# Optimization experiments

Measured on AMD Instinct MI355X. Metric: run time of the kernel, lower is better.

The kernel has to match this reference:

```python
import jax, jax.numpy as jnp
import numpy as np

N = 100000      # nodes
E = 1600000     # edges
G = 8           # graphs in batch
H = 128         # hidden_dim
CNN = 768
MORPH = 6
NC = 5
EPS = 1e-5      # BatchNorm eps


def setup_inputs() -> dict:
    key = jax.random.key(0)
    ks = jax.random.split(key, 32)
    D = CNN + MORPH

    def w(k, shape, fan_in):
        # kaiming_normal_ (relu): std = sqrt(2/fan_in)
        return jax.random.normal(k, shape, jnp.float32) * np.sqrt(2.0 / fan_in)

    inp = {
        "cnn_features": jax.random.normal(ks[0], (N, CNN), jnp.float32),
        "morph_features": jax.random.normal(ks[1], (N, MORPH), jnp.float32),
        "cell_edge_index": jax.random.randint(ks[2], (2, E), 0, N, jnp.int32),
        "batch": jnp.sort(jax.random.randint(ks[3], (N,), 0, G, jnp.int32)),
        # GCN layers (weights stored [in, out])
        "gcn1_w": w(ks[4], (D, H), D), "gcn1_b": jnp.zeros((H,), jnp.float32),
        "gcn2_w": w(ks[5], (H, H), H), "gcn2_b": jnp.zeros((H,), jnp.float32),
        "gcn3_w": w(ks[6], (H, H), H), "gcn3_b": jnp.zeros((H,), jnp.float32),
        # BatchNorm affine params (eval mode, running_mean=0 running_var=1)
        "bn1_g": jnp.ones((H,), jnp.float32), "bn1_b": jnp.zeros((H,), jnp.float32),
        "bn2_g": jnp.ones((H,), jnp.float32), "bn2_b": jnp.zeros((H,), jnp.float32),
        "bn3_g": jnp.ones((H,), jnp.float32), "bn3_b": jnp.zeros((H,), jnp.float32),
        # attention gate: Linear(H,H) -> tanh -> Linear(H,1)
        "att_w1": w(ks[7], (H, H), H), "att_b1": jnp.zeros((H,), jnp.float32),
        "att_w2": w(ks[8], (H, 1), H), "att_b2": jnp.zeros((1,), jnp.float32),
        # classifier MLP
        "cls_w1": w(ks[9], (H, 2 * H), H), "cls_b1": jnp.zeros((2 * H,), jnp.float32),
        "cbn1_g": jnp.ones((2 * H,), jnp.float32), "cbn1_b": jnp.zeros((2 * H,), jnp.float32),
        "cls_w2": w(ks[10], (2 * H, H), 2 * H), "cls_b2": jnp.zeros((H,), jnp.float32),
        "cbn2_g": jnp.ones((H,), jnp.float32), "cbn2_b": jnp.zeros((H,), jnp.float32),
        "cls_w3": w(ks[11], (H, NC), H), "cls_b3": jnp.zeros((NC,), jnp.float32),
    }
    return inp


def _bn_eval(x, gamma, beta):
    # BatchNorm1d eval: running_mean=0, running_var=1
    return x * (gamma / np.sqrt(1.0 + EPS)) + beta


def _gcn(x, w, b, src, dst, dinv):
    h = x @ w                                   # [N, out]
    norm = dinv[src] * dinv[dst]                # [E]
    msg = h[src] * norm[:, None]                # [E, out]
    agg = jax.ops.segment_sum(msg, dst, num_segments=N)
    agg = agg + h * (dinv * dinv)[:, None]      # self-loop contribution
    return agg + b


def _forward(cnn_features, morph_features,
             gcn1_w, gcn1_b, gcn2_w, gcn2_b, gcn3_w, gcn3_b,
             bn1_g, bn1_b, bn2_g, bn2_b, bn3_g, bn3_b,
             att_w1, att_b1, att_w2, att_b2,
             cls_w1, cls_b1, cbn1_g, cbn1_b,
             cls_w2, cls_b2, cbn2_g, cbn2_b,
             cls_w3, cls_b3,
             cell_edge_index, batch):
    x = jnp.concatenate([cnn_features, morph_features], axis=1)  # [N, 774]
    src, dst = cell_edge_index[0], cell_edge_index[1]
    # symmetric GCN normalization with self-loops: deg = in-degree + 1
    deg = jax.ops.segment_sum(jnp.ones((E,), x.dtype), dst, num_segments=N) + 1.0
    dinv = jax.lax.rsqrt(deg)

    x1 = jax.nn.relu(_bn_eval(_gcn(x, gcn1_w, gcn1_b, src, dst, dinv), bn1_g, bn1_b))
    x2 = jax.nn.relu(_bn_eval(_gcn(x1, gcn2_w, gcn2_b, src, dst, dinv), bn2_g, bn2_b))
    x3 = jax.nn.relu(_bn_eval(_gcn(x2, gcn3_w, gcn3_b, src, dst, dinv), bn3_g, bn3_b))
    x_out = x1 + x2 + x3                                        # [N, H]

    # GlobalAttention pooling: segment softmax over per-graph nodes
    gate = jnp.tanh(x_out @ att_w1 + att_b1) @ att_w2 + att_b2  # [N, 1]
    gate = gate[:, 0]
    gmax = jax.ops.segment_max(gate, batch, num_segments=G)
    a = jnp.exp(gate - gmax[batch])
    denom = jax.ops.segment_sum(a, batch, num_segments=G)
    alpha = a / denom[batch]
    pooled = jax.ops.segment_sum(alpha[:, None] * x_out, batch, num_segments=G)  # [G, H]

    # classifier (dropout off, BN eval)
    h = jax.nn.relu(_bn_eval(pooled @ cls_w1 + cls_b1, cbn1_g, cbn1_b))
    h = jax.nn.relu(_bn_eval(h @ cls_w2 + cls_b2, cbn2_g, cbn2_b))
    return h @ cls_w3 + cls_b3                                  # [G, NC]


def reference(cnn_features, morph_features, cell_edge_index, batch,
              gcn1_w, gcn1_b, gcn2_w, gcn2_b, gcn3_w, gcn3_b,
              bn1_g, bn1_b, bn2_g, bn2_b, bn3_g, bn3_b,
              att_w1, att_b1, att_w2, att_b2,
              cls_w1, cls_b1, cbn1_g, cbn1_b,
              cls_w2, cls_b2, cbn2_g, cbn2_b,
              cls_w3, cls_b3):
    return _forward(cnn_features, morph_features,
                    gcn1_w, gcn1_b, gcn2_w, gcn2_b, gcn3_w, gcn3_b,
                    bn1_g, bn1_b, bn2_g, bn2_b, bn3_g, bn3_b,
                    att_w1, att_b1, att_w2, att_b2,
                    cls_w1, cls_b1, cbn1_g, cbn1_b,
                    cls_w2, cls_b2, cbn2_g, cbn2_b,
                    cls_w3, cls_b3,
                    cell_edge_index, batch)
```

## Files before the change

kernel.cpp:

```cpp
#include <hip/hip_runtime.h>
#include <hip/hip_bf16.h>

#define EPSV 1e-5f

typedef short short8v __attribute__((ext_vector_type(8)));
typedef float f32x4 __attribute__((ext_vector_type(4)));

__device__ __forceinline__ unsigned short f2bf(float f){
  unsigned u = __float_as_uint(f);
  unsigned r = u + 0x7fffu + ((u >> 16) & 1u);
  return (unsigned short)(r >> 16);
}
__device__ __forceinline__ unsigned pk2bf(float x, float y){
  return (unsigned)f2bf(x) | ((unsigned)f2bf(y) << 16);
}
__device__ __forceinline__ float bflo(unsigned u){ return __uint_as_float(u << 16); }
__device__ __forceinline__ float bfhi(unsigned u){ return __uint_as_float(u & 0xffff0000u); }

__device__ __forceinline__ unsigned enc_f(float f){
  unsigned u = __float_as_uint(f);
  return (u & 0x80000000u) ? ~u : (u | 0x80000000u);
}
__device__ __forceinline__ float dec_f(unsigned k){
  unsigned u = (k & 0x80000000u) ? (k & 0x7fffffffu) : ~k;
  return __uint_as_float(u);
}

__global__ void hist_kernel(const int* __restrict__ dst, int* __restrict__ deg, int E){
  int i = blockIdx.x*256 + threadIdx.x;
  if (i < E) atomicAdd(&deg[dst[i]], 1);
}

__global__ void scan_partial(const int* __restrict__ deg, int* __restrict__ bsums, int N){
  __shared__ int sd[256];
  int t = threadIdx.x;
  int base = blockIdx.x*1024 + t*4;
  int s = 0;
  if (base+0 < N) s += deg[base+0];
  if (base+1 < N) s += deg[base+1];
  if (base+2 < N) s += deg[base+2];
  if (base+3 < N) s += deg[base+3];
  sd[t]=s; __syncthreads();
  for (int off=128; off>0; off>>=1){
    if (t<off) sd[t]+=sd[t+off];
    __syncthreads();
  }
  if (t==0) bsums[blockIdx.x]=sd[0];
}

__global__ void scan_bsums(int* bsums, int* row_start, int B, int N, int E){
  if (threadIdx.x==0 && blockIdx.x==0){
    int run=0;
    for (int b=0;b<B;b++){ int v=bsums[b]; bsums[b]=run; run+=v; }
    row_start[N]=E;
  }
}

__global__ void scan_final(const int* __restrict__ deg, const int* __restrict__ bsums,
                           int* __restrict__ row_start, int* __restrict__ cursor, int N){
  __shared__ int sd[256];
  int t=threadIdx.x, b=blockIdx.x;
  int base=b*1024+t*4;
  int v0=0,v1=0,v2=0,v3=0;
  if (base+0<N) v0=deg[base+0];
  if (base+1<N) v1=deg[base+1];
  if (base+2<N) v2=deg[base+2];
  if (base+3<N) v3=deg[base+3];
  int s=v0+v1+v2+v3;
  sd[t]=s; __syncthreads();
  for (int off=1; off<256; off<<=1){
    int x = (t>=off)?sd[t-off]:0;
    __syncthreads();
    sd[t]+=x;
    __syncthreads();
  }
  int excl = sd[t]-s + bsums[b];
  int e0=excl, e1=excl+v0, e2=e1+v1, e3=e2+v2;
  if (base+0<N){ row_start[base+0]=e0; cursor[base+0]=e0; }
  if (base+1<N){ row_start[base+1]=e1; cursor[base+1]=e1; }
  if (base+2<N){ row_start[base+2]=e2; cursor[base+2]=e2; }
  if (base+3<N){ row_start[base+3]=e3; cursor[base+3]=e3; }
}

__global__ void dinv_kernel(const int* __restrict__ deg, float* __restrict__ dinv, int N){
  int i = blockIdx.x*256 + threadIdx.x;
  if (i < N) dinv[i] = rsqrtf((float)deg[i] + 1.0f);
}

__global__ void scatter_kernel(const int* __restrict__ src, const int* __restrict__ dst,
                               int* __restrict__ cursor, int* __restrict__ csr_src, int E){
  int i = blockIdx.x*256 + threadIdx.x;
  if (i < E){
    int d = dst[i];
    int pos = atomicAdd(&cursor[d], 1);
    csr_src[pos] = src[i];
  }
}

__global__ void wsplit_kernel(const float* __restrict__ W, unsigned short* __restrict__ WT,
                              int D, int Dpad){
  int k = blockIdx.x*256 + threadIdx.x;
  int c = blockIdx.y;
  if (k >= Dpad) return;
  float v = (k < D) ? W[(size_t)k*128 + c] : 0.f;
  WT[(size_t)c*Dpad + k] = f2bf(v);
}

__global__ __launch_bounds__(256, 4) void gemm_mfma_kernel(
    const float* __restrict__ xa, const float* __restrict__ xb,
    const unsigned short* __restrict__ WT,
    unsigned short* __restrict__ outb, int N, int Da, int Db, int Dpad)
{
  __shared__ unsigned short Abf[128*64];
  __shared__ unsigned short Bbf[128*64];

  const int tid  = threadIdx.x;
  const int lane = tid & 63;
  const int wave = tid >> 6;
  const int lr   = lane & 15;
  const int kg   = lane >> 4;
  const int rowBase = blockIdx.x * 128;
  const int D = Da + Db;

  f32x4 acc[2][8];
  #pragma unroll
  for (int s=0;s<2;s++)
    #pragma unroll
    for (int c=0;c<8;c++){ acc[s][c][0]=0.f; acc[s][c][1]=0.f; acc[s][c][2]=0.f; acc[s][c][3]=0.f; }

  const int arow = tid >> 1;
  const int akseg = (tid & 1) * 32;
  const int Rst = rowBase + arow;

  for (int kc = 0; kc < Dpad; kc += 64){
    __syncthreads();
    {
      const int gk0 = kc + akseg;
      const bool fastA = (Rst < N) && (gk0 + 32 <= Da);
      const int abase = arow*128 + akseg*2;
      const int aswz = (arow & 7) << 4;
      if (fastA){
        const float4* p4 = (const float4*)(xa + (size_t)Rst*Da + gk0);
        #pragma unroll
        for (int s=0;s<4;s++){
          float4 va = p4[2*s];
          float4 vb = p4[2*s+1];
          unsigned u[4];
          u[0] = pk2bf(va.x, va.y); u[1] = pk2bf(va.z, va.w);
          u[2] = pk2bf(vb.x, vb.y); u[3] = pk2bf(vb.z, vb.w);
          int off = (abase + s*16) ^ aswz;
          *(uint4*)((char*)Abf + off) = *(const uint4*)u;
        }
      } else {
        #pragma unroll
        for (int s=0;s<4;s++){
          unsigned u[4];
          #pragma unroll
          for (int q=0;q<4;q++){
            int gk = gk0 + s*8 + 2*q;
            float vx=0.f, vy=0.f;
            if (Rst < N){
              if (gk < Da) vx = xa[(size_t)Rst*Da + gk];
              else if (gk < D) vx = xb[(size_t)Rst*Db + (gk - Da)];
              if (gk+1 < Da) vy = xa[(size_t)Rst*Da + gk+1];
              else if (gk+1 < D) vy = xb[(size_t)Rst*Db + (gk+1 - Da)];
            }
            u[q] = pk2bf(vx, vy);
          }
          int off = (abase + s*16) ^ aswz;
          *(uint4*)((char*)Abf + off) = *(const uint4*)u;
        }
      }
    }
    {
      const unsigned short* ph = WT + (size_t)(tid>>1)*Dpad + kc + akseg;
      const int bbase = (tid>>1)*128 + akseg*2;
      const int bswz = ((tid>>1) & 7) << 4;
      #pragma unroll
      for (int s=0;s<4;s++){
        uint4 h = *(const uint4*)(ph + s*8);
        int off = (bbase + s*16) ^ bswz;
        *(uint4*)((char*)Bbf + off) = h;
      }
    }
    __syncthreads();
    #pragma unroll
    for (int ks=0; ks<2; ks++){
      const int kb = ks*64 + kg*16;
      const int r0 = wave*32 + lr;
      const int r1 = r0 + 16;
      const int offA0 = (r0*128 + kb) ^ ((r0&7)<<4);
      const int offA1 = (r1*128 + kb) ^ ((r1&7)<<4);
      short8v a0 = *(const short8v*)((const char*)Abf + offA0);
      short8v a1 = *(const short8v*)((const char*)Abf + offA1);
      #pragma unroll
      for (int ct=0; ct<8; ct++){
        const int c = ct*16 + lr;
        const int offB = (c*128 + kb) ^ ((c&7)<<4);
        short8v b = *(const short8v*)((const char*)Bbf + offB);
        acc[0][ct] = __builtin_amdgcn_mfma_f32_16x16x32_bf16(a0, b, acc[0][ct], 0,0,0);
        acc[1][ct] = __builtin_amdgcn_mfma_f32_16x16x32_bf16(a1, b, acc[1][ct], 0,0,0);
      }
    }
  }
  const int wrow = rowBase + wave*32;
  #pragma unroll
  for (int strip=0; strip<2; strip++){
    #pragma unroll
    for (int ct=0; ct<8; ct++){
      #pragma unroll
      for (int i=0;i<4;i++){
        int R = wrow + strip*16 + kg*4 + i;
        int C = ct*16 + lr;
        if (R < N) outb[(size_t)R*128 + C] = f2bf(acc[strip][ct][i]);
      }
    }
  }
}

#define ROWFMA(ACC, XV) \
  ACC.x = __builtin_fmaf((XV), w.x, ACC.x); \
  ACC.y = __builtin_fmaf((XV), w.y, ACC.y); \
  ACC.z = __builtin_fmaf((XV), w.z, ACC.z); \
  ACC.w = __builtin_fmaf((XV), w.w, ACC.w);

#define FMA_STEP(K) { \
  const float4 w   = *(const float4*)(Wl + (K)*128 + wb); \
  const float4 xlo = *(const float4*)(Xl + (K)*64 + r0); \
  const float4 xhi = *(const float4*)(Xl + (K)*64 + r0 + 4); \
  ROWFMA(acc0, xlo.x) ROWFMA(acc1, xlo.y) ROWFMA(acc2, xlo.z) ROWFMA(acc3, xlo.w) \
  ROWFMA(acc4, xhi.x) ROWFMA(acc5, xhi.y) ROWFMA(acc6, xhi.z) ROWFMA(acc7, xhi.w) }

#define GEMM_LOOP \
  const int tid  = threadIdx.x; \
  const int lane = tid & 63; \
  const int wave = tid >> 6; \
  const int half = lane >> 5; \
  const int ff   = lane & 31; \
  const int r0   = wave*16 + half*8; \
  const int wb   = ff << 2; \
  const int srow = tid >> 2; \
  const int skg  = (tid & 3) << 4; \
  const int R_s  = rowBase + srow; \
  float4 acc0={0,0,0,0},acc1={0,0,0,0},acc2={0,0,0,0},acc3={0,0,0,0}; \
  float4 acc4={0,0,0,0},acc5={0,0,0,0},acc6={0,0,0,0},acc7={0,0,0,0}; \
  for (int kc = 0; kc < D; kc += 64){ \
    const int L = (D - kc < 64) ? (D - kc) : 64; \
    __syncthreads(); \
    { \
      const int nf4 = (L*128) >> 2; \
      const float4* Wg = (const float4*)(W + (size_t)kc*128); \
      float4* Wl4 = (float4*)Wl; \
      for (int idx = tid; idx < nf4; idx += 256) Wl4[idx] = Wg[idx]; \
    } \
    if (L == 64 && kc + 64 <= Da){ \
      float4 v0={0,0,0,0},v1={0,0,0,0},v2={0,0,0,0},v3={0,0,0,0}; \
      if (R_s < N){ \
        const float4* xr = (const float4*)(xa + (size_t)R_s*Da + kc + skg); \
        v0 = xr[0]; v1 = xr[1]; v2 = xr[2]; v3 = xr[3]; \
      } \
      Xl[(skg+ 0)*64 + srow]=v0.x; Xl[(skg+ 1)*64 + srow]=v0.y; \
      Xl[(skg+ 2)*64 + srow]=v0.z; Xl[(skg+ 3)*64 + srow]=v0.w; \
      Xl[(skg+ 4)*64 + srow]=v1.x; Xl[(skg+ 5)*64 + srow]=v1.y; \
      Xl[(skg+ 6)*64 + srow]=v1.z; Xl[(skg+ 7)*64 + srow]=v1.w; \
      Xl[(skg+ 8)*64 + srow]=v2.x; Xl[(skg+ 9)*64 + srow]=v2.y; \
      Xl[(skg+10)*64 + srow]=v2.z; Xl[(skg+11)*64 + srow]=v2.w; \
      Xl[(skg+12)*64 + srow]=v3.x; Xl[(skg+13)*64 + srow]=v3.y; \
      Xl[(skg+14)*64 + srow]=v3.z; Xl[(skg+15)*64 + srow]=v3.w; \
    } else if (skg < L){ \
      const int lim = (L - skg < 16) ? (L - skg) : 16; \
      for (int i2=0;i2<lim;i2++){ \
        const int gk = kc + skg + i2; \
        float v = 0.f; \
        if (R_s < N) v = (gk < Da) ? xa[(size_t)R_s*Da + gk] \
                                   : xb[(size_t)R_s*Db + (gk - Da)]; \
        Xl[(skg+i2)*64 + srow] = v; \
      } \
    } \
    __syncthreads(); \
    if (L == 64){ \
      _Pragma("unroll 4") \
      for (int k=0;k<64;k++){ FMA_STEP(k) } \
    } else { \
      for (int k=0;k<L;k++){ FMA_STEP(k) } \
    } \
  }

__global__ __launch_bounds__(256) void att_kernel(
    const float* __restrict__ xa, const float* __restrict__ W,
    const float* __restrict__ b1, const float* __restrict__ w2,
    const float* __restrict__ b2, float* __restrict__ gate, int N)
{
  __shared__ float Wl[64*128];
  __shared__ float Xl[64*64];
  const int rowBase = blockIdx.x*64;
  const float* xb = xa;
  const int D = 128, Da = 128, Db = 0;
  GEMM_LOOP
  const int R0 = rowBase + r0;
  const float4 b1v = *(const float4*)(b1 + (ff<<2));
  const float4 w2v = *(const float4*)(w2 + (ff<<2));
  const float bias2 = b2[0];
#define ATT_ROW(ACC, RR) { \
    float p = tanhf(ACC.x + b1v.x)*w2v.x + tanhf(ACC.y + b1v.y)*w2v.y \
            + tanhf(ACC.z + b1v.z)*w2v.z + tanhf(ACC.w + b1v.w)*w2v.w; \
    p += __shfl_xor(p, 1);  p += __shfl_xor(p, 2); \
    p += __shfl_xor(p, 4);  p += __shfl_xor(p, 8); \
    p += __shfl_xor(p, 16); \
    if (ff == 0){ int R = R0 + (RR); if (R < N) gate[R] = p + bias2; } }
  ATT_ROW(acc0,0) ATT_ROW(acc1,1) ATT_ROW(acc2,2) ATT_ROW(acc3,3)
  ATT_ROW(acc4,4) ATT_ROW(acc5,5) ATT_ROW(acc6,6) ATT_ROW(acc7,7)
#undef ATT_ROW
}

__global__ __launch_bounds__(256) void gather_kernel(
    const unsigned short* __restrict__ hb, const float* __restrict__ dinv,
    const int* __restrict__ row_start, const int* __restrict__ csr_src,
    const float* __restrict__ bias, const float* __restrict__ bng, const float* __restrict__ bnb,
    const float* __restrict__ x1in, const float* __restrict__ x2in,
    float* __restrict__ out, int N, int mode)
{
  const int grp = (blockIdx.x * 256 + threadIdx.x) >> 4;
  const int sl  = threadIdx.x & 15;
  if (grp >= N) return;
  const int i = grp;
  const float di = dinv[i];

  float a[8];
  {
    uint4 u = *(const uint4*)(hb + (size_t)i*128 + sl*8);
    float w0 = di*di;
    a[0] = bflo(u.x)*w0; a[1] = bfhi(u.x)*w0;
    a[2] = bflo(u.y)*w0; a[3] = bfhi(u.y)*w0;
    a[4] = bflo(u.z)*w0; a[5] = bfhi(u.z)*w0;
    a[6] = bflo(u.w)*w0; a[7] = bfhi(u.w)*w0;
  }
  const int s0 = row_start[i], s1 = row_start[i+1];
  for (int base = s0; base < s1; base += 16){
    const int nloc = (s1 - base < 16) ? (s1 - base) : 16;
    int sv = 0; float nv = 0.f;
    if (sl < nloc){ sv = csr_src[base + sl]; nv = dinv[sv]*di; }
    for (int j=0;j<nloc;j++){
      int   sj = __shfl(sv, j, 16);
      float nj = __shfl(nv, j, 16);
      uint4 u = *(const uint4*)(hb + (size_t)sj*128 + sl*8);
      a[0] = __builtin_fmaf(bflo(u.x), nj, a[0]);
      a[1] = __builtin_fmaf(bfhi(u.x), nj, a[1]);
      a[2] = __builtin_fmaf(bflo(u.y), nj, a[2]);
      a[3] = __builtin_fmaf(bfhi(u.y), nj, a[3]);
      a[4] = __builtin_fmaf(bflo(u.z), nj, a[4]);
      a[5] = __builtin_fmaf(bfhi(u.z), nj, a[5]);
      a[6] = __builtin_fmaf(bflo(u.w), nj, a[6]);
      a[7] = __builtin_fmaf(bfhi(u.w), nj, a[7]);
    }
  }
  const int f0 = sl*8;
  const float bsc = rsqrtf(1.0f + EPSV);
  float4 bi0 = *(const float4*)(bias + f0);
  float4 bi1 = *(const float4*)(bias + f0 + 4);
  float4 g0 = *(const float4*)(bng + f0);
  float4 g1 = *(const float4*)(bng + f0 + 4);
  float4 be0 = *(const float4*)(bnb + f0);
  float4 be1 = *(const float4*)(bnb + f0 + 4);
  float v[8];
  v[0] = fmaxf(0.f, (a[0]+bi0.x)*(g0.x*bsc) + be0.x);
  v[1] = fmaxf(0.f, (a[1]+bi0.y)*(g0.y*bsc) + be0.y);
  v[2] = fmaxf(0.f, (a[2]+bi0.z)*(g0.z*bsc) + be0.z);
  v[3] = fmaxf(0.f, (a[3]+bi0.w)*(g0.w*bsc) + be0.w);
  v[4] = fmaxf(0.f, (a[4]+bi1.x)*(g1.x*bsc) + be1.x);
  v[5] = fmaxf(0.f, (a[5]+bi1.y)*(g1.y*bsc) + be1.y);
  v[6] = fmaxf(0.f, (a[6]+bi1.z)*(g1.z*bsc) + be1.z);
  v[7] = fmaxf(0.f, (a[7]+bi1.w)*(g1.w*bsc) + be1.w);
  if (mode == 2){
    float4 p0 = *(const float4*)(x1in + (size_t)i*128 + f0);
    float4 p1 = *(const float4*)(x1in + (size_t)i*128 + f0 + 4);
    float4 q0 = *(const float4*)(x2in + (size_t)i*128 + f0);
    float4 q1 = *(const float4*)(x2in + (size_t)i*128 + f0 + 4);
    v[0]+=p0.x+q0.x; v[1]+=p0.y+q0.y; v[2]+=p0.z+q0.z; v[3]+=p0.w+q0.w;
    v[4]+=p1.x+q1.x; v[5]+=p1.y+q1.y; v[6]+=p1.z+q1.z; v[7]+=p1.w+q1.w;
  }
  float4 o0; o0.x=v[0]; o0.y=v[1]; o0.z=v[2]; o0.w=v[3];
  float4 o1; o1.x=v[4]; o1.y=v[5]; o1.z=v[6]; o1.w=v[7];
  *(float4*)(out + (size_t)i*128 + f0)     = o0;
  *(float4*)(out + (size_t)i*128 + f0 + 4) = o1;
}

__global__ void segmax_kernel(const float* __restrict__ gate, const int* __restrict__ batch,
                              unsigned* __restrict__ mg, int N){
  __shared__ unsigned sm[8];
  int t = threadIdx.x;
  if (t < 8) sm[t] = 0u;
  __syncthreads();
  int i = blockIdx.x*256 + t;
  if (i < N) atomicMax(&sm[batch[i]], enc_f(gate[i]));
  __syncthreads();
  if (t < 8) atomicMax(&mg[t], sm[t]);
}

__global__ void expsum_kernel(const float* __restrict__ gate, const int* __restrict__ batch,
                              const unsigned* __restrict__ mg, float* __restrict__ aex,
                              float* __restrict__ denom, int N){
  __shared__ float sd[8];
  int t = threadIdx.x;
  if (t < 8) sd[t] = 0.f;
  __syncthreads();
  int i = blockIdx.x*256 + t;
  if (i < N){
    int g = batch[i];
    float m = dec_f(mg[g]);
    float av = expf(gate[i] - m);
    aex[i] = av;
    atomicAdd(&sd[g], av);
  }
  __syncthreads();
  if (t < 8) atomicAdd(&denom[t], sd[t]);
}

__global__ void pooled_kernel(const float* __restrict__ aex, const float* __restrict__ xo,
                              const int* __restrict__ batch, float* __restrict__ pooled, int N){
  int t = threadIdx.x;
  int hlf = t >> 7;
  int f = t & 127;
  int nb = gridDim.x;
  int per = (N + nb - 1)/nb;
  int start = blockIdx.x*per;
  int end = (N < start + per) ? N : (start + per);
  float acc = 0.f; int gcur = -1;
  for (int i = start + hlf; i < end; i += 2){
    int g = batch[i];
    if (g != gcur){
      if (gcur >= 0) atomicAdd(&pooled[gcur*128 + f], acc);
      acc = 0.f; gcur = g;
    }
    acc = __builtin_fmaf(aex[i], xo[(size_t)i*128 + f], acc);
  }
  if (gcur >= 0) atomicAdd(&pooled[gcur*128 + f], acc);
}

__global__ __launch_bounds__(256) void classifier_kernel(
    const float* __restrict__ pooled, const float* __restrict__ denom,
    const float* __restrict__ w1, const float* __restrict__ b1,
    const float* __restrict__ g1, const float* __restrict__ be1,
    const float* __restrict__ w2, const float* __restrict__ b2,
    const float* __restrict__ g2, const float* __restrict__ be2,
    const float* __restrict__ w3, const float* __restrict__ b3,
    float* __restrict__ outp)
{
  __shared__ float pl[8*128];
  __shared__ float h1[8*256];
  __shared__ float h2l[8*128];
  int t = threadIdx.x;
  for (int idx = t; idx < 1024; idx += 256){
    int g = idx >> 7;
    pl[idx] = pooled[idx] / denom[g];
  }
  __syncthreads();
  {
    float a0=0,a1=0,a2=0,a3=0,a4=0,a5=0,a6=0,a7=0;
    for (int k=0; k<128; k++){
      float w = w1[k*256 + t];
      a0 = __builtin_fmaf(pl[0*128+k], w, a0);
      a1 = __builtin_fmaf(pl[1*128+k], w, a1);
      a2 = __builtin_fmaf(pl[2*128+k], w, a2);
      a3 = __builtin_fmaf(pl[3*128+k], w, a3);
      a4 = __builtin_fmaf(pl[4*128+k], w, a4);
      a5 = __builtin_fmaf(pl[5*128+k], w, a5);
      a6 = __builtin_fmaf(pl[6*128+k], w, a6);
      a7 = __builtin_fmaf(pl[7*128+k], w, a7);
// ... 33 lines not shown
    h2l[5*128+t] = fmaxf(0.f, (a5+bb)*s + tb);
    h2l[6*128+t] = fmaxf(0.f, (a6+bb)*s + tb);
    h2l[7*128+t] = fmaxf(0.f, (a7+bb)*s + tb);
  }
  __syncthreads();
  if (t < 40){
    int g = t/5, c = t%5;
    float s = 0.f;
    for (int k=0; k<128; k++) s = __builtin_fmaf(h2l[g*128+k], w3[k*5+c], s);
    outp[t] = s + b3[c];
  }
}

extern "C" void kernel_launch(void* const* d_in, const int* in_sizes, int n_in,
                              void* d_out, int out_size, void* d_ws, size_t ws_size,
                              hipStream_t stream)
{
  const float* cnn   = (const float*)d_in[0];
  const float* morph = (const float*)d_in[1];
  const int*   eidx  = (const int*)d_in[2];
  const int*   batch = (const int*)d_in[3];
  const float* g1w = (const float*)d_in[4];
  const float* g1b = (const float*)d_in[5];
  const float* g2w = (const float*)d_in[6];
  const float* g2b = (const float*)d_in[7];
  const float* g3w = (const float*)d_in[8];
  const float* g3b = (const float*)d_in[9];
  const float* bn1g=(const float*)d_in[10], *bn1b=(const float*)d_in[11];
  const float* bn2g=(const float*)d_in[12], *bn2b=(const float*)d_in[13];
  const float* bn3g=(const float*)d_in[14], *bn3b=(const float*)d_in[15];
  const float* aw1=(const float*)d_in[16], *ab1=(const float*)d_in[17];
  const float* aw2=(const float*)d_in[18], *ab2=(const float*)d_in[19];
  const float* cw1=(const float*)d_in[20], *cb1=(const float*)d_in[21];
  const float* c1g=(const float*)d_in[22], *c1b=(const float*)d_in[23];
  const float* cw2=(const float*)d_in[24], *cb2=(const float*)d_in[25];
  const float* c2g=(const float*)d_in[26], *c2b=(const float*)d_in[27];
  const float* cw3=(const float*)d_in[28], *cb3=(const float*)d_in[29];

  const int N = in_sizes[3];
  const int E = in_sizes[2] / 2;
  const int CNNW = in_sizes[0] / N;
  const int MOR  = in_sizes[1] / N;
  const int D = CNNW + MOR;
  const int Dpad1 = ((D + 63)/64)*64;

  char* p = (char*)d_ws;
  auto alloc = [&](size_t bytes)->char* {
    char* r = p; p += (bytes + 255) & ~(size_t)255; return r;
  };
  unsigned short* hbuf = (unsigned short*)alloc((size_t)N*128*2);
  float* x1    = (float*)alloc((size_t)N*128*4);
  float* x2    = (float*)alloc((size_t)N*128*4);
  float* dinv  = (float*)alloc((size_t)N*4);
  float* gate  = (float*)alloc((size_t)N*4);
  float* aex   = (float*)alloc((size_t)N*4);
  char* zstart = p;
  int* deg      = (int*)alloc((size_t)N*4);
  unsigned* mg  = (unsigned*)alloc(8*4);
  float* denom  = (float*)alloc(8*4);
  float* pooled = (float*)alloc(8*128*4);
  size_t zbytes = (size_t)(p - zstart);
  int* row_start=(int*)alloc((size_t)(N+1)*4);
  int* cursor  = (int*)alloc((size_t)N*4);
  int* csr_src = (int*)alloc((size_t)E*4);
  int* bsums   = (int*)alloc(4096);
  unsigned short* w1T = (unsigned short*)alloc((size_t)128*Dpad1*2);
  unsigned short* w2T = (unsigned short*)alloc((size_t)128*128*2);
  unsigned short* w3T = (unsigned short*)alloc((size_t)128*128*2);

  hipMemsetAsync(zstart, 0, zbytes, stream);

  const int* srcp = eidx;
  const int* dstp = eidx + E;

  int gE = (E + 255)/256;
  int gN = (N + 255)/256;
  int B  = (N + 1023)/1024;
  int gMfma = (N + 127)/128;
  int gAtt  = (N + 63)/64;
  int gGat  = (N + 15)/16;

  hist_kernel<<<dim3(gE), dim3(256), 0, stream>>>(dstp, deg, E);
  scan_partial<<<dim3(B), dim3(256), 0, stream>>>(deg, bsums, N);
  scan_bsums<<<dim3(1), dim3(64), 0, stream>>>(bsums, row_start, B, N, E);
  scan_final<<<dim3(B), dim3(256), 0, stream>>>(deg, bsums, row_start, cursor, N);
  dinv_kernel<<<dim3(gN), dim3(256), 0, stream>>>(deg, dinv, N);
  scatter_kernel<<<dim3(gE), dim3(256), 0, stream>>>(srcp, dstp, cursor, csr_src, E);

  wsplit_kernel<<<dim3((Dpad1+255)/256, 128), dim3(256), 0, stream>>>(g1w, w1T, D, Dpad1);
  wsplit_kernel<<<dim3(1, 128), dim3(256), 0, stream>>>(g2w, w2T, 128, 128);
  wsplit_kernel<<<dim3(1, 128), dim3(256), 0, stream>>>(g3w, w3T, 128, 128);

  gemm_mfma_kernel<<<dim3(gMfma), dim3(256), 0, stream>>>(cnn, morph, w1T, hbuf, N, CNNW, MOR, Dpad1);
  gather_kernel<<<dim3(gGat), dim3(256), 0, stream>>>(hbuf, dinv, row_start, csr_src,
      g1b, bn1g, bn1b, (const float*)nullptr, (const float*)nullptr, x1, N, 0);
  gemm_mfma_kernel<<<dim3(gMfma), dim3(256), 0, stream>>>(x1, (const float*)nullptr, w2T, hbuf, N, 128, 0, 128);
  gather_kernel<<<dim3(gGat), dim3(256), 0, stream>>>(hbuf, dinv, row_start, csr_src,
      g2b, bn2g, bn2b, (const float*)nullptr, (const float*)nullptr, x2, N, 0);
  gemm_mfma_kernel<<<dim3(gMfma), dim3(256), 0, stream>>>(x2, (const float*)nullptr, w3T, hbuf, N, 128, 0, 128);
  gather_kernel<<<dim3(gGat), dim3(256), 0, stream>>>(hbuf, dinv, row_start, csr_src,
      g3b, bn3g, bn3b, x1, x2, x1, N, 2);

  att_kernel<<<dim3(gAtt), dim3(256), 0, stream>>>(x1, aw1, ab1, aw2, ab2, gate, N);
  segmax_kernel<<<dim3(gN), dim3(256), 0, stream>>>(gate, batch, mg, N);
  expsum_kernel<<<dim3(gN), dim3(256), 0, stream>>>(gate, batch, mg, aex, denom, N);
  pooled_kernel<<<dim3(512), dim3(256), 0, stream>>>(aex, x1, batch, pooled, N);

  classifier_kernel<<<dim3(1), dim3(256), 0, stream>>>(pooled, denom,
      cw1, cb1, c1g, c1b, cw2, cb2, c2g, c2b, cw3, cb3, (float*)d_out);
}
```

Before: 750.6 us.

## Fuse attention softmax into MFMA gate kernel, prefetch GEMM tiles, unroll gather

```diff
diff --git a/kernel.cpp b/kernel.cpp
--- a/kernel.cpp
+++ b/kernel.cpp
@@ -14,17 +14,11 @@
 __device__ __forceinline__ unsigned pk2bf(float x, float y){
   return (unsigned)f2bf(x) | ((unsigned)f2bf(y) << 16);
 }
+__device__ __forceinline__ float bf2f(unsigned short s){
+  return __uint_as_float(((unsigned)s) << 16);
+}
 __device__ __forceinline__ float bflo(unsigned u){ return __uint_as_float(u << 16); }
 __device__ __forceinline__ float bfhi(unsigned u){ return __uint_as_float(u & 0xffff0000u); }
-
-__device__ __forceinline__ unsigned enc_f(float f){
-  unsigned u = __float_as_uint(f);
-  return (u & 0x80000000u) ? ~u : (u | 0x80000000u);
-}
-__device__ __forceinline__ float dec_f(unsigned k){
-  unsigned u = (k & 0x80000000u) ? (k & 0x7fffffffu) : ~k;
-  return __uint_as_float(u);
-}
 
 __global__ void hist_kernel(const int* __restrict__ dst, int* __restrict__ deg, int E){
   int i = blockIdx.x*256 + threadIdx.x;
@@ -57,7 +51,8 @@
 }
 
 __global__ void scan_final(const int* __restrict__ deg, const int* __restrict__ bsums,
-                           int* __restrict__ row_start, int* __restrict__ cursor, int N){
+                           int* __restrict__ row_start, int* __restrict__ cursor,
+                           float* __restrict__ dinv, int N){
   __shared__ int sd[256];
   int t=threadIdx.x, b=blockIdx.x;
   int base=b*1024+t*4;
@@ -76,15 +71,10 @@
   }
   int excl = sd[t]-s + bsums[b];
   int e0=excl, e1=excl+v0, e2=e1+v1, e3=e2+v2;
-  if (base+0<N){ row_start[base+0]=e0; cursor[base+0]=e0; }
-  if (base+1<N){ row_start[base+1]=e1; cursor[base+1]=e1; }
-  if (base+2<N){ row_start[base+2]=e2; cursor[base+2]=e2; }
-  if (base+3<N){ row_start[base+3]=e3; cursor[base+3]=e3; }
-}
-
-__global__ void dinv_kernel(const int* __restrict__ deg, float* __restrict__ dinv, int N){
-  int i = blockIdx.x*256 + threadIdx.x;
-  if (i < N) dinv[i] = rsqrtf((float)deg[i] + 1.0f);
+  if (base+0<N){ row_start[base+0]=e0; cursor[base+0]=e0; dinv[base+0]=rsqrtf((float)v0+1.0f); }
+  if (base+1<N){ row_start[base+1]=e1; cursor[base+1]=e1; dinv[base+1]=rsqrtf((float)v1+1.0f); }
+  if (base+2<N){ row_start[base+2]=e2; cursor[base+2]=e2; dinv[base+2]=rsqrtf((float)v2+1.0f); }
+  if (base+3<N){ row_start[base+3]=e3; cursor[base+3]=e3; dinv[base+3]=rsqrtf((float)v3+1.0f); }
 }
 
 __global__ void scatter_kernel(const int* __restrict__ src, const int* __restrict__ dst,
@@ -106,7 +96,49 @@
   WT[(size_t)c*Dpad + k] = f2bf(v);
 }
 
-__global__ __launch_bounds__(256, 4) void gemm_mfma_kernel(
+__global__ void wsplit_all(const float* __restrict__ W2, const float* __restrict__ W3,
+                           const float* __restrict__ WA,
+                           unsigned short* __restrict__ w2T, unsigned short* __restrict__ w3T,
+                           unsigned short* __restrict__ aT_hi, unsigned short* __restrict__ aT_lo){
+  int k = threadIdx.x;
+  int c = blockIdx.y;
+  int z = blockIdx.z;
+  if (z == 0){
+    w2T[c*128 + k] = f2bf(W2[(size_t)k*128 + c]);
+  } else if (z == 1){
+    w3T[c*128 + k] = f2bf(W3[(size_t)k*128 + c]);
+  } else {
+    float v = WA[(size_t)k*128 + c];
+    unsigned short h = f2bf(v);
+    aT_hi[c*128 + k] = h;
+    aT_lo[c*128 + k] = f2bf(v - bf2f(h));
+  }
+}
+
+#define LOADA(KC) { \
+  const int gk0 = (KC) + akseg; \
+  if ((Rst < N) && (gk0 + 32 <= Da)){ \
+    const float4* p4 = (const float4*)(xa + (size_t)Rst*Da + gk0); \
+    pa0=p4[0]; pa1=p4[1]; pa2=p4[2]; pa3=p4[3]; pa4=p4[4]; pa5=p4[5]; pa6=p4[6]; pa7=p4[7]; \
+  } else { \
+    float tmp[32]; \
+    _Pragma("unroll") \
+    for (int q=0;q<32;q++){ \
+      int gk = gk0 + q; float x = 0.f; \
+      if (Rst < N){ \
+        if (gk < Da) x = xa[(size_t)Rst*Da + gk]; \
+        else if (gk < D) x = xb[(size_t)Rst*Db + (gk - Da)]; \
+      } \
+      tmp[q]=x; } \
+    pa0=*(float4*)&tmp[0];  pa1=*(float4*)&tmp[4];  pa2=*(float4*)&tmp[8];  pa3=*(float4*)&tmp[12]; \
+    pa4=*(float4*)&tmp[16]; pa5=*(float4*)&tmp[20]; pa6=*(float4*)&tmp[24]; pa7=*(float4*)&tmp[28]; \
+  } }
+
+#define LOADW(KC) { \
+  const unsigned short* ph = wrowp + (KC); \
+  pw0=*(const uint4*)(ph); pw1=*(const uint4*)(ph+8); pw2=*(const uint4*)(ph+16); pw3=*(const uint4*)(ph+24); }
+
+__global__ __launch_bounds__(256, 3) void gemm_mfma_kernel(
     const float* __restrict__ xa, const float* __restrict__ xb,
     const unsigned short* __restrict__ WT,
     unsigned short* __restrict__ outb, int N, int Da, int Db, int Dpad)
@@ -131,59 +163,39 @@
   const int arow = tid >> 1;
   const int akseg = (tid & 1) * 32;
   const int Rst = rowBase + arow;
+  const int abase = arow*128 + akseg*2;
+  const int aswz  = (arow & 7) << 4;
+  const unsigned short* wrowp = WT + (size_t)arow*Dpad + akseg;
+
+  float4 pa0,pa1,pa2,pa3,pa4,pa5,pa6,pa7;
+  uint4  pw0,pw1,pw2,pw3;
+
+  LOADA(0)
+  LOADW(0)
 
   for (int kc = 0; kc < Dpad; kc += 64){
     __syncthreads();
     {
-      const int gk0 = kc + akseg;
-      const bool fastA = (Rst < N) && (gk0 + 32 <= Da);
-      const int abase = arow*128 + akseg*2;
-      const int aswz = (arow & 7) << 4;
-      if (fastA){
-        const float4* p4 = (const float4*)(xa + (size_t)Rst*Da + gk0);
-        #pragma unroll
-        for (int s=0;s<4;s++){
-          float4 va = p4[2*s];
-          float4 vb = p4[2*s+1];
-          unsigned u[4];
-          u[0] = pk2bf(va.x, va.y); u[1] = pk2bf(va.z, va.w);
-          u[2] = pk2bf(vb.x, vb.y); u[3] = pk2bf(vb.z, vb.w);
-          int off = (abase + s*16) ^ aswz;
-          *(uint4*)((char*)Abf + off) = *(const uint4*)u;
-        }
-      } else {
-        #pragma unroll
-        for (int s=0;s<4;s++){
-          unsigned u[4];
-          #pragma unroll
-          for (int q=0;q<4;q++){
-            int gk = gk0 + s*8 + 2*q;
-            float vx=0.f, vy=0.f;
-            if (Rst < N){
-              if (gk < Da) vx = xa[(size_t)Rst*Da + gk];
-              else if (gk < D) vx = xb[(size_t)Rst*Db + (gk - Da)];
-              if (gk+1 < Da) vy = xa[(size_t)Rst*Da + gk+1];
-              else if (gk+1 < D) vy = xb[(size_t)Rst*Db + (gk+1 - Da)];
-            }
-            u[q] = pk2bf(vx, vy);
-          }
-          int off = (abase + s*16) ^ aswz;
-          *(uint4*)((char*)Abf + off) = *(const uint4*)u;
-        }
-      }
-    }
-    {
-      const unsigned short* ph = WT + (size_t)(tid>>1)*Dpad + kc + akseg;
-      const int bbase = (tid>>1)*128 + akseg*2;
-      const int bswz = ((tid>>1) & 7) << 4;
-      #pragma unroll
-      for (int s=0;s<4;s++){
-        uint4 h = *(const uint4*)(ph + s*8);
-        int off = (bbase + s*16) ^ bswz;
-        *(uint4*)((char*)Bbf + off) = h;
-      }
+      unsigned u[4];
+      u[0]=pk2bf(pa0.x,pa0.y); u[1]=pk2bf(pa0.z,pa0.w); u[2]=pk2bf(pa1.x,pa1.y); u[3]=pk2bf(pa1.z,pa1.w);
+      *(uint4*)((char*)Abf + ((abase+ 0)^aswz)) = *(const uint4*)u;
+      u[0]=pk2bf(pa2.x,pa2.y); u[1]=pk2bf(pa2.z,pa2.w); u[2]=pk2bf(pa3.x,pa3.y); u[3]=pk2bf(pa3.z,pa3.w);
+      *(uint4*)((char*)Abf + ((abase+16)^aswz)) = *(const uint4*)u;
+      u[0]=pk2bf(pa4.x,pa4.y); u[1]=pk2bf(pa4.z,pa4.w); u[2]=pk2bf(pa5.x,pa5.y); u[3]=pk2bf(pa5.z,pa5.w);
+      *(uint4*)((char*)Abf + ((abase+32)^aswz)) = *(const uint4*)u;
+      u[0]=pk2bf(pa6.x,pa6.y); u[1]=pk2bf(pa6.z,pa6.w); u[2]=pk2bf(pa7.x,pa7.y); u[3]=pk2bf(pa7.z,pa7.w);
+      *(uint4*)((char*)Abf + ((abase+48)^aswz)) = *(const uint4*)u;
+      *(uint4*)((char*)Bbf + ((abase+ 0)^aswz)) = pw0;
+      *(uint4*)((char*)Bbf + ((abase+16)^aswz)) = pw1;
+      *(uint4*)((char*)Bbf + ((abase+32)^aswz)) = pw2;
+      *(uint4*)((char*)Bbf + ((abase+48)^aswz)) = pw3;
     }
     __syncthreads();
+    const int kn = kc + 64;
+    if (kn < Dpad){
+      LOADA(kn)
+      LOADW(kn)
+    }
     #pragma unroll
     for (int ks=0; ks<2; ks++){
       const int kb = ks*64 + kg*16;
@@ -218,100 +230,145 @@
   }
 }
 
-#define ROWFMA(ACC, XV) \
-  ACC.x = __builtin_fmaf((XV), w.x, ACC.x); \
-  ACC.y = __builtin_fmaf((XV), w.y, ACC.y); \
-  ACC.z = __builtin_fmaf((XV), w.z, ACC.z); \
-  ACC.w = __builtin_fmaf((XV), w.w, ACC.w);
-
-#define FMA_STEP(K) { \
-  const float4 w   = *(const float4*)(Wl + (K)*128 + wb); \
-  const float4 xlo = *(const float4*)(Xl + (K)*64 + r0); \
-  const float4 xhi = *(const float4*)(Xl + (K)*64 + r0 + 4); \
-  ROWFMA(acc0, xlo.x) ROWFMA(acc1, xlo.y) ROWFMA(acc2, xlo.z) ROWFMA(acc3, xlo.w) \
-  ROWFMA(acc4, xhi.x) ROWFMA(acc5, xhi.y) ROWFMA(acc6, xhi.z) ROWFMA(acc7, xhi.w) }
-
-#define GEMM_LOOP \
-  const int tid  = threadIdx.x; \
-  const int lane = tid & 63; \
-  const int wave = tid >> 6; \
-  const int half = lane >> 5; \
-  const int ff   = lane & 31; \
-  const int r0   = wave*16 + half*8; \
-  const int wb   = ff << 2; \
-  const int srow = tid >> 2; \
-  const int skg  = (tid & 3) << 4; \
-  const int R_s  = rowBase + srow; \
-  float4 acc0={0,0,0,0},acc1={0,0,0,0},acc2={0,0,0,0},acc3={0,0,0,0}; \
-  float4 acc4={0,0,0,0},acc5={0,0,0,0},acc6={0,0,0,0},acc7={0,0,0,0}; \
-  for (int kc = 0; kc < D; kc += 64){ \
-    const int L = (D - kc < 64) ? (D - kc) : 64; \
-    __syncthreads(); \
-    { \
-      const int nf4 = (L*128) >> 2; \
-      const float4* Wg = (const float4*)(W + (size_t)kc*128); \
-      float4* Wl4 = (float4*)Wl; \
-      for (int idx = tid; idx < nf4; idx += 256) Wl4[idx] = Wg[idx]; \
-    } \
-    if (L == 64 && kc + 64 <= Da){ \
-      float4 v0={0,0,0,0},v1={0,0,0,0},v2={0,0,0,0},v3={0,0,0,0}; \
-      if (R_s < N){ \
-        const float4* xr = (const float4*)(xa + (size_t)R_s*Da + kc + skg); \
-        v0 = xr[0]; v1 = xr[1]; v2 = xr[2]; v3 = xr[3]; \
-      } \
-      Xl[(skg+ 0)*64 + srow]=v0.x; Xl[(skg+ 1)*64 + srow]=v0.y; \
-      Xl[(skg+ 2)*64 + srow]=v0.z; Xl[(skg+ 3)*64 + srow]=v0.w; \
-      Xl[(skg+ 4)*64 + srow]=v1.x; Xl[(skg+ 5)*64 + srow]=v1.y; \
-      Xl[(skg+ 6)*64 + srow]=v1.z; Xl[(skg+ 7)*64 + srow]=v1.w; \
-      Xl[(skg+ 8)*64 + srow]=v2.x; Xl[(skg+ 9)*64 + srow]=v2.y; \
-      Xl[(skg+10)*64 + srow]=v2.z; Xl[(skg+11)*64 + srow]=v2.w; \
-      Xl[(skg+12)*64 + srow]=v3.x; Xl[(skg+13)*64 + srow]=v3.y; \
-      Xl[(skg+14)*64 + srow]=v3.z; Xl[(skg+15)*64 + srow]=v3.w; \
-    } else if (skg < L){ \
-      const int lim = (L - skg < 16) ? (L - skg) : 16; \
-      for (int i2=0;i2<lim;i2++){ \
-        const int gk = kc + skg + i2; \
-        float v = 0.f; \
-        if (R_s < N) v = (gk < Da) ? xa[(size_t)R_s*Da + gk] \
-                                   : xb[(size_t)R_s*Db + (gk - Da)]; \
-        Xl[(skg+i2)*64 + srow] = v; \
-      } \
-    } \
-    __syncthreads(); \
-    if (L == 64){ \
-      _Pragma("unroll 4") \
-      for (int k=0;k<64;k++){ FMA_STEP(k) } \
-    } else { \
-      for (int k=0;k<L;k++){ FMA_STEP(k) } \
-    } \
-  }
-
-__global__ __launch_bounds__(256) void att_kernel(
-    const float* __restrict__ xa, const float* __restrict__ W,
-    const float* __restrict__ b1, const float* __restrict__ w2,
-    const float* __restrict__ b2, float* __restrict__ gate, int N)
+__global__ __launch_bounds__(256) void att_mfma_kernel(
+    const float* __restrict__ xa,
+    const unsigned short* __restrict__ WhiT, const unsigned short* __restrict__ WloT,
+    const float* __restrict__ b1, const float* __restrict__ w2, const float* __restrict__ b2,
+    const int* __restrict__ batch,
+    float* __restrict__ aex, float* __restrict__ denom, int N)
 {
-  __shared__ float Wl[64*128];
-  __shared__ float Xl[64*64];
-  const int rowBase = blockIdx.x*64;
-  const float* xb = xa;
-  const int D = 128, Da = 128, Db = 0;
-  GEMM_LOOP
-  const int R0 = rowBase + r0;
-  const float4 b1v = *(const float4*)(b1 + (ff<<2));
-  const float4 w2v = *(const float4*)(w2 + (ff<<2));
+  __shared__ unsigned short Ahi[128*64];
+  __shared__ unsigned short Alo[128*64];
+  __shared__ unsigned short Bhi[128*64];
+  __shared__ unsigned short Blo[128*64];
+  __shared__ float sden[8];
+
+  const int tid  = threadIdx.x;
+  const int lane = tid & 63;
+  const int wave = tid >> 6;
+  const int lr   = lane & 15;
+  const int kg   = lane >> 4;
+  const int rowBase = blockIdx.x * 128;
+
+  if (tid < 8) sden[tid] = 0.f;
+
+  f32x4 acc[2][8];
+  #pragma unroll
+  for (int s=0;s<2;s++)
+    #pragma unroll
+    for (int c=0;c<8;c++){ acc[s][c][0]=0.f; acc[s][c][1]=0.f; acc[s][c][2]=0.f; acc[s][c][3]=0.f; }
+
+  const int arow = tid >> 1;
+  const int akseg = (tid & 1) * 32;
+  const int Rst = rowBase + arow;
+  const int abase = arow*128 + akseg*2;
+  const int aswz  = (arow & 7) << 4;
+
+  for (int kc = 0; kc < 128; kc += 64){
+    __syncthreads();
+    {
+      const int gk0 = kc + akseg;
+      float4 v0={0,0,0,0},v1={0,0,0,0},v2={0,0,0,0},v3={0,0,0,0};
+      float4 v4={0,0,0,0},v5={0,0,0,0},v6={0,0,0,0},v7={0,0,0,0};
+      if (Rst < N){
+        const float4* p4 = (const float4*)(xa + (size_t)Rst*128 + gk0);
+        v0=p4[0]; v1=p4[1]; v2=p4[2]; v3=p4[3]; v4=p4[4]; v5=p4[5]; v6=p4[6]; v7=p4[7];
+      }
+#define STAGE_HL(VA, VB, SOFF) { \
+      unsigned uh[4], ul[4]; \
+      unsigned short h0=f2bf(VA.x), h1=f2bf(VA.y), h2=f2bf(VA.z), h3=f2bf(VA.w); \
+      unsigned short h4=f2bf(VB.x), h5=f2bf(VB.y), h6=f2bf(VB.z), h7=f2bf(VB.w); \
+      uh[0]=(unsigned)h0|((unsigned)h1<<16); uh[1]=(unsigned)h2|((unsigned)h3<<16); \
+      uh[2]=(unsigned)h4|((unsigned)h5<<16); uh[3]=(unsigned)h6|((unsigned)h7<<16); \
+      ul[0]=pk2bf(VA.x-bf2f(h0), VA.y-bf2f(h1)); ul[1]=pk2bf(VA.z-bf2f(h2), VA.w-bf2f(h3)); \
+      ul[2]=pk2bf(VB.x-bf2f(h4), VB.y-bf2f(h5)); ul[3]=pk2bf(VB.z-bf2f(h6), VB.w-bf2f(h7)); \
+      *(uint4*)((char*)Ahi + ((abase+(SOFF))^aswz)) = *(const uint4*)uh; \
+      *(uint4*)((char*)Alo + ((abase+(SOFF))^aswz)) = *(const uint4*)ul; }
+      STAGE_HL(v0, v1,  0)
+      STAGE_HL(v2, v3, 16)
+      STAGE_HL(v4, v5, 32)
+      STAGE_HL(v6, v7, 48)
+#undef STAGE_HL
+    }
+    {
+      const unsigned short* ph = WhiT + (size_t)arow*128 + kc + akseg;
+      const unsigned short* pl = WloT + (size_t)arow*128 + kc + akseg;
+      *(uint4*)((char*)Bhi + ((abase+ 0)^aswz)) = *(const uint4*)(ph);
+      *(uint4*)((char*)Bhi + ((abase+16)^aswz)) = *(const uint4*)(ph+8);
+      *(uint4*)((char*)Bhi + ((abase+32)^aswz)) = *(const uint4*)(ph+16);
+      *(uint4*)((char*)Bhi + ((abase+48)^aswz)) = *(const uint4*)(ph+24);
+      *(uint4*)((char*)Blo + ((abase+ 0)^aswz)) = *(const uint4*)(pl);
+      *(uint4*)((char*)Blo + ((abase+16)^aswz)) = *(const uint4*)(pl+8);
+      *(uint4*)((char*)Blo + ((abase+32)^aswz)) = *(const uint4*)(pl+16);
+      *(uint4*)((char*)Blo + ((abase+48)^aswz)) = *(const uint4*)(pl+24);
+    }
+    __syncthreads();
+    #pragma unroll
+    for (int ks=0; ks<2; ks++){
+      const int kb = ks*64 + kg*16;
+      const int r0 = wave*32 + lr;
+      const int r1 = r0 + 16;
+      const int offA0 = (r0*128 + kb) ^ ((r0&7)<<4);
+      const int offA1 = (r1*128 + kb) ^ ((r1&7)<<4);
+      short8v ah0 = *(const short8v*)((const char*)Ahi + offA0);
+      short8v al0 = *(const short8v*)((const char*)Alo + offA0);
+      short8v ah1 = *(const short8v*)((const char*)Ahi + offA1);
+      short8v al1 = *(const short8v*)((const char*)Alo + offA1);
+      #pragma unroll
+      for (int ct=0; ct<8; ct++){
+        const int c = ct*16 + lr;
+        const int offB = (c*128 + kb) ^ ((c&7)<<4);
+        short8v bh = *(const short8v*)((const char*)Bhi + offB);
+        short8v bl = *(const short8v*)((const char*)Blo + offB);
+        acc[0][ct] = __builtin_amdgcn_mfma_f32_16x16x32_bf16(ah0, bh, acc[0][ct], 0,0,0);
+        acc[0][ct] = __builtin_amdgcn_mfma_f32_16x16x32_bf16(ah0, bl, acc[0][ct], 0,0,0);
+        acc[0][ct] = __builtin_amdgcn_mfma_f32_16x16x32_bf16(al0, bh, acc[0][ct], 0,0,0);
+        acc[1][ct] = __builtin_amdgcn_mfma_f32_16x16x32_bf16(ah1, bh, acc[1][ct], 0,0,0);
+        acc[1][ct] = __builtin_amdgcn_mfma_f32_16x16x32_bf16(ah1, bl, acc[1][ct], 0,0,0);
+        acc[1][ct] = __builtin_amdgcn_mfma_f32_16x16x32_bf16(al1, bh, acc[1][ct], 0,0,0);
+      }
+    }
+  }
+  float b1v[8], w2v[8];
+  #pragma unroll
+  for (int ct=0; ct<8; ct++){
+    b1v[ct] = b1[ct*16 + lr];
+    w2v[ct] = w2[ct*16 + lr];
+  }
   const float bias2 = b2[0];
-#define ATT_ROW(ACC, RR) { \
-    float p = tanhf(ACC.x + b1v.x)*w2v.x + tanhf(ACC.y + b1v.y)*w2v.y \
-            + tanhf(ACC.z + b1v.z)*w2v.z + tanhf(ACC.w + b1v.w)*w2v.w; \
-    p += __shfl_xor(p, 1);  p += __shfl_xor(p, 2); \
-    p += __shfl_xor(p, 4);  p += __shfl_xor(p, 8); \
-    p += __shfl_xor(p, 16); \
-    if (ff == 0){ int R = R0 + (RR); if (R < N) gate[R] = p + bias2; } }
-  ATT_ROW(acc0,0) ATT_ROW(acc1,1) ATT_ROW(acc2,2) ATT_ROW(acc3,3)
-  ATT_ROW(acc4,4) ATT_ROW(acc5,5) ATT_ROW(acc6,6) ATT_ROW(acc7,7)
-#undef ATT_ROW
-}
+  const int wrow = rowBase + wave*32;
+  #pragma unroll
+  for (int strip=0; strip<2; strip++){
+    #pragma unroll
+    for (int i=0;i<4;i++){
+      float p = 0.f;
+      #pragma unroll
+      for (int ct=0; ct<8; ct++){
+        p += tanhf(acc[strip][ct][i] + b1v[ct]) * w2v[ct];
+      }
+      p += __shfl_xor(p, 1, 16);
+      p += __shfl_xor(p, 2, 16);
+      p += __shfl_xor(p, 4, 16);
+      p += __shfl_xor(p, 8, 16);
+      if (lr == 0){
+        int R = wrow + strip*16 + kg*4 + i;
+        if (R < N){
+          float e = expf(p + bias2);
+          aex[R] = e;
+          atomicAdd(&sden[batch[R]], e);
+        }
+      }
+    }
+  }
+  __syncthreads();
+  if (tid < 8 && sden[tid] != 0.f) atomicAdd(&denom[tid], sden[tid]);
+}
+
+#define GFMA8(U, NJ) \
+  a0=__builtin_fmaf(bflo(U.x),(NJ),a0); a1=__builtin_fmaf(bfhi(U.x),(NJ),a1); \
+  a2=__builtin_fmaf(bflo(U.y),(NJ),a2); a3=__builtin_fmaf(bfhi(U.y),(NJ),a3); \
+  a4=__builtin_fmaf(bflo(U.z),(NJ),a4); a5=__builtin_fmaf(bfhi(U.z),(NJ),a5); \
+  a6=__builtin_fmaf(bflo(U.w),(NJ),a6); a7=__builtin_fmaf(bfhi(U.w),(NJ),a7);
 
 __global__ __launch_bounds__(256) void gather_kernel(
     const unsigned short* __restrict__ hb, const float* __restrict__ dinv,
@@ -325,33 +382,50 @@
   if (grp >= N) return;
   const int i = grp;
   const float di = dinv[i];
-
-  float a[8];
+  const uint4* __restrict__ h4 = (const uint4*)hb;
+
+  float a0,a1,a2,a3,a4,a5,a6,a7;
   {
-    uint4 u = *(const uint4*)(hb + (size_t)i*128 + sl*8);
+    uint4 u = h4[(size_t)i*16 + sl];
     float w0 = di*di;
-    a[0] = bflo(u.x)*w0; a[1] = bfhi(u.x)*w0;
-    a[2] = bflo(u.y)*w0; a[3] = bfhi(u.y)*w0;
-    a[4] = bflo(u.z)*w0; a[5] = bfhi(u.z)*w0;
-    a[6] = bflo(u.w)*w0; a[7] = bfhi(u.w)*w0;
-  }
-  const int s0 = row_start[i], s1 = row_start[i+1];
-  for (int base = s0; base < s1; base += 16){
-    const int nloc = (s1 - base < 16) ? (s1 - base) : 16;
+    a0=bflo(u.x)*w0; a1=bfhi(u.x)*w0; a2=bflo(u.y)*w0; a3=bfhi(u.y)*w0;
+    a4=bflo(u.z)*w0; a5=bfhi(u.z)*w0; a6=bflo(u.w)*w0; a7=bfhi(u.w)*w0;
+  }
+  int base = row_start[i];
+  const int s1 = row_start[i+1];
+  while (base + 16 <= s1){
+    int sv = csr_src[base + sl];
+    float nv = dinv[sv]*di;
+    #pragma unroll
+    for (int j=0; j<16; j+=4){
+      int sj0 = __shfl(sv, j,   16);
+      int sj1 = __shfl(sv, j+1, 16);
+      int sj2 = __shfl(sv, j+2, 16);
+      int sj3 = __shfl(sv, j+3, 16);
+      float nj0 = __shfl(nv, j,   16);
+      float nj1 = __shfl(nv, j+1, 16);
+      float nj2 = __shfl(nv, j+2, 16);
+      float nj3 = __shfl(nv, j+3, 16);
+      uint4 u0 = h4[(size_t)sj0*16 + sl];
+      uint4 u1 = h4[(size_t)sj1*16 + sl];
+      uint4 u2 = h4[(size_t)sj2*16 + sl];
+      uint4 u3 = h4[(size_t)sj3*16 + sl];
+      GFMA8(u0, nj0)
+      GFMA8(u1, nj1)
+      GFMA8(u2, nj2)
+      GFMA8(u3, nj3)
+    }
+    base += 16;
+  }
+  const int rem = s1 - base;
+  if (rem > 0){
     int sv = 0; float nv = 0.f;
-    if (sl < nloc){ sv = csr_src[base + sl]; nv = dinv[sv]*di; }
-    for (int j=0;j<nloc;j++){
+    if (sl < rem){ sv = csr_src[base + sl]; nv = dinv[sv]*di; }
+    for (int j=0; j<rem; j++){
       int   sj = __shfl(sv, j, 16);
       float nj = __shfl(nv, j, 16);
-      uint4 u = *(const uint4*)(hb + (size_t)sj*128 + sl*8);
-      a[0] = __builtin_fmaf(bflo(u.x), nj, a[0]);
-      a[1] = __builtin_fmaf(bfhi(u.x), nj, a[1]);
-      a[2] = __builtin_fmaf(bflo(u.y), nj, a[2]);
-      a[3] = __builtin_fmaf(bfhi(u.y), nj, a[3]);
-      a[4] = __builtin_fmaf(bflo(u.z), nj, a[4]);
-      a[5] = __builtin_fmaf(bfhi(u.z), nj, a[5]);
-      a[6] = __builtin_fmaf(bflo(u.w), nj, a[6]);
-      a[7] = __builtin_fmaf(bfhi(u.w), nj, a[7]);
+      uint4 u = h4[(size_t)sj*16 + sl];
+      GFMA8(u, nj)
     }
   }
   const int f0 = sl*8;
@@ -363,14 +437,14 @@
   float4 be0 = *(const float4*)(bnb + f0);
   float4 be1 = *(const float4*)(bnb + f0 + 4);
   float v[8];
-  v[0] = fmaxf(0.f, (a[0]+bi0.x)*(g0.x*bsc) + be0.x);
-  v[1] = fmaxf(0.f, (a[1]+bi0.y)*(g0.y*bsc) + be0.y);
-  v[2] = fmaxf(0.f, (a[2]+bi0.z)*(g0.z*bsc) + be0.z);
-  v[3] = fmaxf(0.f, (a[3]+bi0.w)*(g0.w*bsc) + be0.w);
-  v[4] = fmaxf(0.f, (a[4]+bi1.x)*(g1.x*bsc) + be1.x);
-  v[5] = fmaxf(0.f, (a[5]+bi1.y)*(g1.y*bsc) + be1.y);
-  v[6] = fmaxf(0.f, (a[6]+bi1.z)*(g1.z*bsc) + be1.z);
-  v[7] = fmaxf(0.f, (a[7]+bi1.w)*(g1.w*bsc) + be1.w);
+  v[0] = fmaxf(0.f, (a0+bi0.x)*(g0.x*bsc) + be0.x);
+  v[1] = fmaxf(0.f, (a1+bi0.y)*(g0.y*bsc) + be0.y);
+  v[2] = fmaxf(0.f, (a2+bi0.z)*(g0.z*bsc) + be0.z);
+  v[3] = fmaxf(0.f, (a3+bi0.w)*(g0.w*bsc) + be0.w);
+  v[4] = fmaxf(0.f, (a4+bi1.x)*(g1.x*bsc) + be1.x);
+  v[5] = fmaxf(0.f, (a5+bi1.y)*(g1.y*bsc) + be1.y);
+  v[6] = fmaxf(0.f, (a6+bi1.z)*(g1.z*bsc) + be1.z);
+  v[7] = fmaxf(0.f, (a7+bi1.w)*(g1.w*bsc) + be1.w);
   if (mode == 2){
     float4 p0 = *(const float4*)(x1in + (size_t)i*128 + f0);
     float4 p1 = *(const float4*)(x1in + (size_t)i*128 + f0 + 4);
@@ -383,37 +457,6 @@
   float4 o1; o1.x=v[4]; o1.y=v[5]; o1.z=v[6]; o1.w=v[7];
   *(float4*)(out + (size_t)i*128 + f0)     = o0;
   *(float4*)(out + (size_t)i*128 + f0 + 4) = o1;
-}
-
-__global__ void segmax_kernel(const float* __restrict__ gate, const int* __restrict__ batch,
-                              unsigned* __restrict__ mg, int N){
-  __shared__ unsigned sm[8];
-  int t = threadIdx.x;
-  if (t < 8) sm[t] = 0u;
-  __syncthreads();
-  int i = blockIdx.x*256 + t;
-  if (i < N) atomicMax(&sm[batch[i]], enc_f(gate[i]));
-  __syncthreads();
-  if (t < 8) atomicMax(&mg[t], sm[t]);
-}
-
-__global__ void expsum_kernel(const float* __restrict__ gate, const int* __restrict__ batch,
-                              const unsigned* __restrict__ mg, float* __restrict__ aex,
-                              float* __restrict__ denom, int N){
-  __shared__ float sd[8];
-  int t = threadIdx.x;
-  if (t < 8) sd[t] = 0.f;
-  __syncthreads();
-  int i = blockIdx.x*256 + t;
-  if (i < N){
-    int g = batch[i];
-    float m = dec_f(mg[g]);
-    float av = expf(gate[i] - m);
-    aex[i] = av;
-    atomicAdd(&sd[g], av);
-  }
-  __syncthreads();
-  if (t < 8) atomicAdd(&denom[t], sd[t]);
 }
 
 __global__ void pooled_kernel(const float* __restrict__ aex, const float* __restrict__ xo,
@@ -553,11 +596,9 @@
   float* x1    = (float*)alloc((size_t)N*128*4);
   float* x2    = (float*)alloc((size_t)N*128*4);
   float* dinv  = (float*)alloc((size_t)N*4);
-  float* gate  = (float*)alloc((size_t)N*4);
   float* aex   = (float*)alloc((size_t)N*4);
   char* zstart = p;
   int* deg      = (int*)alloc((size_t)N*4);
-  unsigned* mg  = (unsigned*)alloc(8*4);
   float* denom  = (float*)alloc(8*4);
   float* pooled = (float*)alloc(8*128*4);
   size_t zbytes = (size_t)(p - zstart);
@@ -568,6 +609,8 @@
   unsigned short* w1T = (unsigned short*)alloc((size_t)128*Dpad1*2);
   unsigned short* w2T = (unsigned short*)alloc((size_t)128*128*2);
   unsigned short* w3T = (unsigned short*)alloc((size_t)128*128*2);
+  unsigned short* aw1hiT = (unsigned short*)alloc((size_t)128*128*2);
+  unsigned short* aw1loT = (unsigned short*)alloc((size_t)128*128*2);
 
   hipMemsetAsync(zstart, 0, zbytes, stream);
 
@@ -575,22 +618,18 @@
   const int* dstp = eidx + E;
 
   int gE = (E + 255)/256;
-  int gN = (N + 255)/256;
   int B  = (N + 1023)/1024;
   int gMfma = (N + 127)/128;
-  int gAtt  = (N + 63)/64;
   int gGat  = (N + 15)/16;
 
   hist_kernel<<<dim3(gE), dim3(256), 0, stream>>>(dstp, deg, E);
   scan_partial<<<dim3(B), dim3(256), 0, stream>>>(deg, bsums, N);
   scan_bsums<<<dim3(1), dim3(64), 0, stream>>>(bsums, row_start, B, N, E);
-  scan_final<<<dim3(B), dim3(256), 0, stream>>>(deg, bsums, row_start, cursor, N);
-  dinv_kernel<<<dim3(gN), dim3(256), 0, stream>>>(deg, dinv, N);
+  scan_final<<<dim3(B), dim3(256), 0, stream>>>(deg, bsums, row_start, cursor, dinv, N);
   scatter_kernel<<<dim3(gE), dim3(256), 0, stream>>>(srcp, dstp, cursor, csr_src, E);
 
   wsplit_kernel<<<dim3((Dpad1+255)/256, 128), dim3(256), 0, stream>>>(g1w, w1T, D, Dpad1);
-  wsplit_kernel<<<dim3(1, 128), dim3(256), 0, stream>>>(g2w, w2T, 128, 128);
-  wsplit_kernel<<<dim3(1, 128), dim3(256), 0, stream>>>(g3w, w3T, 128, 128);
+  wsplit_all<<<dim3(1, 128, 3), dim3(128), 0, stream>>>(g2w, g3w, aw1, w2T, w3T, aw1hiT, aw1loT);
 
   gemm_mfma_kernel<<<dim3(gMfma), dim3(256), 0, stream>>>(cnn, morph, w1T, hbuf, N, CNNW, MOR, Dpad1);
   gather_kernel<<<dim3(gGat), dim3(256), 0, stream>>>(hbuf, dinv, row_start, csr_src,
@@ -602,9 +641,8 @@
   gather_kernel<<<dim3(gGat), dim3(256), 0, stream>>>(hbuf, dinv, row_start, csr_src,
       g3b, bn3g, bn3b, x1, x2, x1, N, 2);
 
-  att_kernel<<<dim3(gAtt), dim3(256), 0, stream>>>(x1, aw1, ab1, aw2, ab2, gate, N);
-  segmax_kernel<<<dim3(gN), dim3(256), 0, stream>>>(gate, batch, mg, N);
-  expsum_kernel<<<dim3(gN), dim3(256), 0, stream>>>(gate, batch, mg, aex, denom, N);
+  att_mfma_kernel<<<dim3(gMfma), dim3(256), 0, stream>>>(x1, aw1hiT, aw1loT,
+      ab1, aw2, ab2, batch, aex, denom, N);
   pooled_kernel<<<dim3(512), dim3(256), 0, stream>>>(aex, x1, batch, pooled, N);
 
   classifier_kernel<<<dim3(1), dim3(256), 0, stream>>>(pooled, denom,
```

Result: no change. 751.3 us (+0.1%).
